# Kernel optimization log

Measured on AMD Instinct MI355X. Metric: run time of the kernel, lower is better.

Reference implementation:

```python
import jax, jax.numpy as jnp
import numpy as np

DT = 1e-3   # timestep (s)
DH = 10.0   # grid spacing (m)


def setup_inputs() -> dict:
    key = jax.random.key(0)
    k1, k2, k3, k4 = jax.random.split(key, 4)
    B, NT, NZ, NX, NREC = 8, 256, 256, 256, 64
    x = jax.random.normal(k1, (B, NT), dtype=jnp.float32)            # source wavelets
    vp = 1500.0 + 2000.0 * jax.random.uniform(k2, (NZ, NX), dtype=jnp.float32)
    src_loc = jax.random.randint(k3, (B, 2), 4, NZ - 4, dtype=jnp.int32)        # (z,x) per shot
    rec_loc = jax.random.randint(k4, (B, NREC, 2), 4, NZ - 4, dtype=jnp.int32)  # (z,x) per rec
    return {"x": x, "vp": vp, "src_loc": src_loc, "rec_loc": rec_loc}


def reference(x, vp, src_loc, rec_loc):
    """Acoustic 2nd-order leapfrog FD time-stepping (WaveRNN pattern):
    per step: stencil update -> source scatter-inject -> receiver gather.
    Returns receiver traces (B, NT, NREC)."""
    B, NT = x.shape
    nz, nx = vp.shape
    c2dt2 = (vp * vp) * jnp.float32(DT * DT)   # (nz, nx), broadcast over batch
    inv_dh2 = jnp.float32(1.0 / (DH * DH))
    bidx = jnp.arange(B)
    sz, sx = src_loc[:, 0], src_loc[:, 1]
    rz, rx = rec_loc[..., 0], rec_loc[..., 1]

    def laplacian(h):  # 5-point stencil, zero (Dirichlet) boundaries
        interior = (h[:, 2:, 1:-1] + h[:, :-2, 1:-1]
                    + h[:, 1:-1, 2:] + h[:, 1:-1, :-2]
                    - 4.0 * h[:, 1:-1, 1:-1]) * inv_dh2
        return jnp.zeros_like(h).at[:, 1:-1, 1:-1].set(interior)

    def step(carry, wav_t):
        h1, h2 = carry                              # fields at t, t-1
        hn = 2.0 * h1 - h2 + c2dt2 * laplacian(h1)  # leapfrog update
        hn = hn.at[bidx, sz, sx].add(jnp.float32(DT * DT) * wav_t)  # source inject
        rec = hn[bidx[:, None], rz, rx]             # receiver gather (B, NREC)
        return (hn, h1), rec

    h0 = jnp.zeros((B, nz, nx), dtype=x.dtype)
    _, recs = jax.lax.scan(step, (h0, h0), x.T)     # recs: (NT, B, NREC)
    return jnp.transpose(recs, (1, 0, 2))           # (B, NT, NREC)
```

## Files before the change

### kernel.cpp

```cpp
#include <hip/hip_runtime.h>

typedef float v4f __attribute__((ext_vector_type(4)));

namespace {
constexpr int B_     = 8;
constexpr int NT_    = 256;
constexpr int NX_    = 256;
constexpr int NREC_  = 64;
constexpr int PIECES = 16;
constexpr int IROWS  = 16;
constexpr int G      = 16;
constexpr int ROUNDS = NT_ / G;
constexpr int NB     = (IROWS + 2 * G) / 4;
constexpr int NTHR   = NB * 64;
constexpr int NBLK   = B_ * PIECES;
constexpr float DT2  = 1e-6f;
constexpr float KLAP = 1e-8f;
constexpr size_t FLAGS_BYTES = 4096;
constexpr int RCAP = 6;
}

__device__ __forceinline__ float dpp_shr1(float v) {
    return __int_as_float(__builtin_amdgcn_update_dpp(
        0, __float_as_int(v), 0x138 , 0xF, 0xF, true));
}
__device__ __forceinline__ float dpp_shl1(float v) {
    return __int_as_float(__builtin_amdgcn_update_dpp(
        0, __float_as_int(v), 0x130 , 0xF, 0xF, true));
}

__device__ __forceinline__ void store_v4_sys(float* p, v4f v) {
    asm volatile("global_store_dwordx4 %0, %1, off sc0 sc1"
                 :: "v"(p), "v"(v) : "memory");
}
__device__ __forceinline__ v4f load_v4_sys(const float* p) {
    v4f r;
    asm volatile("global_load_dwordx4 %0, %1, off sc0 sc1"
                 : "=v"(r) : "v"(p) : "memory");
    return r;
}

extern "C" __global__
__attribute__((amdgpu_flat_work_group_size(NTHR, NTHR), amdgpu_waves_per_eu(4, 4)))
void wave_reg_kernel(const float* __restrict__ x,
                     const float* __restrict__ vp,
                     const int* __restrict__ src_loc,
                     const int* __restrict__ rec_loc,
                     float* __restrict__ out,
                     int* __restrict__ flags,
                     float* __restrict__ gbuf)
{
    __shared__ float pub[3][2][NB][256];
    __shared__ int   prog[NB];
    __shared__ float wav[NT_];
    __shared__ float recbuf[G][NREC_];
    __shared__ unsigned char recown[NREC_];

    const int bid  = blockIdx.x;
    const int b    = bid & 7;
    const int p    = bid >> 3;
    const int blk  = b * PIECES + p;
    const int tid  = threadIdx.x;
    const int band = tid >> 6;
    const int lane = tid & 63;
    const int c0   = lane << 2;
    const int grt  = p * IROWS - G + (band << 2);

    const int cut = (band < 4) ? ((band << 2) + 3)
                  : ((band < 8) ? G : (47 - (band << 2)));

    if (tid < NT_) wav[tid] = x[b * NT_ + tid];
    if (tid < NREC_) {
        int rz = rec_loc[(b * NREC_ + tid) * 2 + 0];
        recown[tid] = (rz >= p * IROWS && rz < p * IROWS + IROWS) ? 1 : 0;
    }

    v4f cf[4], cf2[4];
#pragma unroll
    for (int i = 0; i < 4; ++i) {
        int gr = grt + i;
        int crow = gr < 0 ? 0 : (gr > 255 ? 255 : gr);
        bool rowok = (gr >= 1) && (gr <= 254);
        v4f vv = *(const v4f*)&vp[crow * NX_ + c0];
        float cc[4];
#pragma unroll
        for (int k = 0; k < 4; ++k) {
            int col = c0 + k;
            float vk = (k == 0) ? vv.x : (k == 1) ? vv.y : (k == 2) ? vv.z : vv.w;
            cc[k] = (rowok && col >= 1 && col <= 254) ? vk * vk * KLAP : 0.f;
        }
        cf[i].x = cc[0]; cf[i].y = cc[1]; cf[i].z = cc[2]; cf[i].w = cc[3];
        cf2[i].x = 2.f - 4.f * cc[0]; cf2[i].y = 2.f - 4.f * cc[1];
        cf2[i].z = 2.f - 4.f * cc[2]; cf2[i].w = 2.f - 4.f * cc[3];
    }

    const int sz = src_loc[b * 2 + 0], sx = src_loc[b * 2 + 1];
    const int si = sz - grt;
    const int sj = sx - c0;
    const bool has_src = ((unsigned)si < 4u) && ((unsigned)sj < 4u);
    const bool wave_has_src = __any(has_src);

    int rs[RCAP]; int rcnt = 0;
#pragma unroll 1
    for (int r = 0; r < NREC_; ++r) {
        int rz = rec_loc[(b * NREC_ + r) * 2 + 0];
        int rx = rec_loc[(b * NREC_ + r) * 2 + 1];
        int i = rz - grt, j = rx - c0;
        if (rz >= p * IROWS && rz < p * IROWS + IROWS &&
            (unsigned)i < 4u && (unsigned)j < 4u) {
            if (rcnt < RCAP) rs[rcnt] = (r << 4) | (i << 2) | j;
            ++rcnt;
        }
    }
    if (rcnt > RCAP) rcnt = RCAP;
    const bool wave_has_rec = __any(rcnt > 0);
    float* outb = out + (size_t)b * NT_ * NREC_;

    v4f A[4], Bv[4];
    {
        v4f z = {0.f, 0.f, 0.f, 0.f};
#pragma unroll
        for (int i = 0; i < 4; ++i) { A[i] = z; Bv[i] = z; }
    }

    *(v4f*)&pub[0][0][band][c0] = A[0];
    *(v4f*)&pub[0][1][band][c0] = A[3];
    if (lane == 0) prog[band] = 0;
    __syncthreads();

    auto gptr = [&](int e, int bk, int lvl, int rr) -> float* {
        return gbuf + ((((size_t)(e & 1) * NBLK + bk) * 2 + lvl) * 16 + rr) * 256;
    };

#define ROW(I, NV, SV) do {                                                   \
    float wv = dpp_shr1(C[I].w);       \
    float ev = dpp_shl1(C[I].x);      \
    v4f hn;                                                                   \
    { float sm = ((NV).x + (SV).x) + (wv     + C[I].y);                       \
      hn.x = fmaf(cf[I].x, sm, fmaf(cf2[I].x, C[I].x, -P[I].x)); }            \
    { float sm = ((NV).y + (SV).y) + (C[I].x + C[I].z);                       \
      hn.y = fmaf(cf[I].y, sm, fmaf(cf2[I].y, C[I].y, -P[I].y)); }            \
    { float sm = ((NV).z + (SV).z) + (C[I].y + C[I].w);                       \
      hn.z = fmaf(cf[I].z, sm, fmaf(cf2[I].z, C[I].z, -P[I].z)); }            \
    { float sm = ((NV).w + (SV).w) + (C[I].z + ev);                           \
      hn.w = fmaf(cf[I].w, sm, fmaf(cf2[I].w, C[I].w, -P[I].w)); }            \
    P[I] = hn;                                                                \
} while (0)

    auto step = [&](v4f (&C)[4], v4f (&P)[4], int t, int s3) {
        const int k = (t & (G - 1)) + 1;
        if (k > cut) return;
        const int nxt = (s3 == 2) ? 0 : s3 + 1;
        if (band > 0)
            while (__hip_atomic_load(&prog[band - 1], __ATOMIC_ACQUIRE,
                                     __HIP_MEMORY_SCOPE_WORKGROUP) < t)
                __builtin_amdgcn_s_sleep(1);
        if (band < NB - 1)
            while (__hip_atomic_load(&prog[band + 1], __ATOMIC_ACQUIRE,
                                     __HIP_MEMORY_SCOPE_WORKGROUP) < t)
                __builtin_amdgcn_s_sleep(1);
        v4f nn, ss;
        if (band > 0)      nn = *(const v4f*)&pub[s3][1][band - 1][c0];
        else               { nn.x = 0.f; nn.y = 0.f; nn.z = 0.f; nn.w = 0.f; }
        if (band < NB - 1) ss = *(const v4f*)&pub[s3][0][band + 1][c0];
        else               { ss.x = 0.f; ss.y = 0.f; ss.z = 0.f; ss.w = 0.f; }
        ROW(1, C[0], C[2]);
        ROW(2, C[1], C[3]);
        ROW(0, nn,   C[1]);
        ROW(3, C[2], ss);
        if (wave_has_src) {
            const float sv = DT2 * wav[t];
#pragma unroll
            for (int i = 0; i < 4; ++i) {
                if (has_src && si == i) {
                    if      (sj == 0) P[i].x += sv;
                    else if (sj == 1) P[i].y += sv;
                    else if (sj == 2) P[i].z += sv;
                    else              P[i].w += sv;
                }
            }
        }
        *(v4f*)&pub[nxt][0][band][c0] = P[0];
        *(v4f*)&pub[nxt][1][band][c0] = P[3];
        const int nv = (k == cut && cut < G) ? (t - k + 17)
                                             : (t + 1);
        if (lane == 0)
            __hip_atomic_store(&prog[band], nv, __ATOMIC_RELEASE,
                               __HIP_MEMORY_SCOPE_WORKGROUP);
        if (wave_has_rec) {
#pragma unroll
            for (int kk = 0; kk < RCAP; ++kk) {
                if (rcnt > kk) {
                    int pk = rs[kk];
                    int i = (pk >> 2) & 3, j = pk & 3, r = pk >> 4;
                    v4f t01 = (i & 1) ? P[1] : P[0];
                    v4f t23 = (i & 1) ? P[3] : P[2];
                    v4f rw  = (i & 2) ? t23 : t01;
                    float c01 = (j & 1) ? rw.y : rw.x;
                    float c23 = (j & 1) ? rw.w : rw.z;
                    recbuf[t & (G - 1)][r] = (j & 2) ? c23 : c01;
                }
            }
        }
    };

    auto publish_prev = [&](int e) {
        if (band >= 4 && band < 8) {
            int rr0 = (band - 4) << 2;
#pragma unroll
            for (int i = 0; i < 4; ++i)
                store_v4_sys(&gptr(e, blk, 1, rr0 + i)[c0], Bv[i]);
        }
    };

    auto exchange = [&](int e, int s3) {
        if (band >= 4 && band < 8) {
            int rr0 = (band - 4) << 2;
#pragma unroll
            for (int i = 0; i < 4; ++i)
                store_v4_sys(&gptr(e, blk, 0, rr0 + i)[c0], A[i]);
        }
        __syncthreads();
        if (tid == 0)
            __hip_atomic_store(&flags[blk], e + 1, __ATOMIC_RELAXED,
                               __HIP_MEMORY_SCOPE_SYSTEM);
        if (band < 4 && p > 0) {
            if (lane == 0)
                while (__hip_atomic_load(&flags[blk - 1], __ATOMIC_RELAXED,
                                         __HIP_MEMORY_SCOPE_SYSTEM) < e + 1)
                    __builtin_amdgcn_s_sleep(1);
            int rr0 = band << 2;
#pragma unroll
            for (int i = 0; i < 4; ++i) {
                A[i]  = load_v4_sys(&gptr(e, blk - 1, 0, rr0 + i)[c0]);
                Bv[i] = load_v4_sys(&gptr(e, blk - 1, 1, rr0 + i)[c0]);
            }
        }
        if (band >= 8 && p < PIECES - 1) {
            if (lane == 0)
                while (__hip_atomic_load(&flags[blk + 1], __ATOMIC_RELAXED,
                                         __HIP_MEMORY_SCOPE_SYSTEM) < e + 1)
                    __builtin_amdgcn_s_sleep(1);
            int rr0 = (band - 8) << 2;
#pragma unroll
            for (int i = 0; i < 4; ++i) {
                A[i]  = load_v4_sys(&gptr(e, blk + 1, 0, rr0 + i)[c0]);
                Bv[i] = load_v4_sys(&gptr(e, blk + 1, 1, rr0 + i)[c0]);
            }
        }
        asm volatile("s_waitcnt vmcnt(0)" ::: "memory");
        __builtin_amdgcn_sched_barrier(0);
        *(v4f*)&pub[s3][0][band][c0] = A[0];
        *(v4f*)&pub[s3][1][band][c0] = A[3];
        __syncthreads();
    };

    int t = 0, s3 = 0;
#pragma unroll 1
    for (int e = 0; e < ROUNDS; ++e) {
#pragma unroll 1
        for (int s = 0; s < G; s += 2) {
            step(A, Bv, t, s3);  s3 = (s3 == 2) ? 0 : s3 + 1;
            if (s == G - 2 && e < ROUNDS - 1)
                publish_prev(e);
            step(Bv, A, t + 1, s3); s3 = (s3 == 2) ? 0 : s3 + 1;
            t += 2;
        }
        __syncthreads();
#pragma unroll 1
        for (int idx = tid; idx < G * NREC_; idx += NTHR) {
            int s = idx >> 6, r = idx & 63;
            if (recown[r]) outb[(e * G + s) * NREC_ + r] = recbuf[s][r];
        }
        if (e < ROUNDS - 1) exchange(e, s3);
    }
#undef ROW
}

extern "C" void kernel_launch(void* const* d_in, const int* in_sizes, int n_in,
                              void* d_out, int out_size, void* d_ws, size_t ws_size,
                              hipStream_t stream) {
    const float* x   = (const float*)d_in[0];
    const float* vp  = (const float*)d_in[1];
    const int*   src = (const int*)d_in[2];
    const int*   rec = (const int*)d_in[3];
    float*       o   = (float*)d_out;
    int*   flags = (int*)d_ws;
    float* gbuf  = (float*)((char*)d_ws + FLAGS_BYTES);
    (void)hipMemsetAsync(d_ws, 0, FLAGS_BYTES, stream);
    hipLaunchKernelGGL(wave_reg_kernel, dim3(NBLK), dim3(NTHR), 0, stream,
                       x, vp, src, rec, o, flags, gbuf);
}
```

Baseline: 298.8 us.

## Replace block-wide round barriers with per-band flags and direct receiver stores

Removes the per-round __syncthreads and shared-memory receiver staging. Receivers are now written straight to global memory from the owning wave. Cross-block halo exchange moves from per-block flags to per-band flags, so each interior band publishes its state and each halo band waits only for its own source band. Halo bands resynchronise with their inner neighbour through the existing progress counters instead of a block barrier. This lets bands drift across round boundaries, at the cost of more complex flag and progress bookkeeping and scattered global receiver stores.

```diff
diff --git a/kernel.cpp b/kernel.cpp
--- a/kernel.cpp
+++ b/kernel.cpp
@@ -11,7 +11,7 @@
 constexpr int IROWS  = 16;
 constexpr int G      = 16;
 constexpr int ROUNDS = NT_ / G;
-constexpr int NB     = (IROWS + 2 * G) / 4;
+constexpr int NB     = 12;
 constexpr int NTHR   = NB * 64;
 constexpr int NBLK   = B_ * PIECES;
 constexpr float DT2  = 1e-6f;
@@ -53,8 +53,6 @@
     __shared__ float pub[3][2][NB][256];
     __shared__ int   prog[NB];
     __shared__ float wav[NT_];
-    __shared__ float recbuf[G][NREC_];
-    __shared__ unsigned char recown[NREC_];
 
     const int bid  = blockIdx.x;
     const int b    = bid & 7;
@@ -70,10 +68,6 @@
                   : ((band < 8) ? G : (47 - (band << 2)));
 
     if (tid < NT_) wav[tid] = x[b * NT_ + tid];
-    if (tid < NREC_) {
-        int rz = rec_loc[(b * NREC_ + tid) * 2 + 0];
-        recown[tid] = (rz >= p * IROWS && rz < p * IROWS + IROWS) ? 1 : 0;
-    }
 
     v4f cf[4], cf2[4];
 #pragma unroll
@@ -133,8 +127,8 @@
     };
 
 #define ROW(I, NV, SV) do {                                                   \
-    float wv = dpp_shr1(C[I].w);       \
-    float ev = dpp_shl1(C[I].x);      \
+    float wv = dpp_shr1(C[I].w);                                              \
+    float ev = dpp_shl1(C[I].x);                                              \
     v4f hn;                                                                   \
     { float sm = ((NV).x + (SV).x) + (wv     + C[I].y);                       \
       hn.x = fmaf(cf[I].x, sm, fmaf(cf2[I].x, C[I].x, -P[I].x)); }            \
@@ -147,9 +141,8 @@
     P[I] = hn;                                                                \
 } while (0)
 
-    auto step = [&](v4f (&C)[4], v4f (&P)[4], int t, int s3) {
-        const int k = (t & (G - 1)) + 1;
-        if (k > cut) return;
+    auto step = [&](v4f (&C)[4], v4f (&P)[4], int t) {
+        const int s3  = t % 3;
         const int nxt = (s3 == 2) ? 0 : s3 + 1;
         if (band > 0)
             while (__hip_atomic_load(&prog[band - 1], __ATOMIC_ACQUIRE,
@@ -182,10 +175,8 @@
         }
         *(v4f*)&pub[nxt][0][band][c0] = P[0];
         *(v4f*)&pub[nxt][1][band][c0] = P[3];
-        const int nv = (k == cut && cut < G) ? (t - k + 17)
-                                             : (t + 1);
         if (lane == 0)
-            __hip_atomic_store(&prog[band], nv, __ATOMIC_RELEASE,
+            __hip_atomic_store(&prog[band], t + 1, __ATOMIC_RELEASE,
                                __HIP_MEMORY_SCOPE_WORKGROUP);
         if (wave_has_rec) {
 #pragma unroll
@@ -198,81 +189,68 @@
                     v4f rw  = (i & 2) ? t23 : t01;
                     float c01 = (j & 1) ? rw.y : rw.x;
                     float c23 = (j & 1) ? rw.w : rw.z;
-                    recbuf[t & (G - 1)][r] = (j & 2) ? c23 : c01;
+                    outb[t * NREC_ + r] = (j & 2) ? c23 : c01;
                 }
             }
         }
     };
 
-    auto publish_prev = [&](int e) {
-        if (band >= 4 && band < 8) {
-            int rr0 = (band - 4) << 2;
-#pragma unroll
-            for (int i = 0; i < 4; ++i)
-                store_v4_sys(&gptr(e, blk, 1, rr0 + i)[c0], Bv[i]);
-        }
-    };
-
-    auto exchange = [&](int e, int s3) {
-        if (band >= 4 && band < 8) {
-            int rr0 = (band - 4) << 2;
-#pragma unroll
-            for (int i = 0; i < 4; ++i)
-                store_v4_sys(&gptr(e, blk, 0, rr0 + i)[c0], A[i]);
-        }
-        __syncthreads();
-        if (tid == 0)
-            __hip_atomic_store(&flags[blk], e + 1, __ATOMIC_RELAXED,
-                               __HIP_MEMORY_SCOPE_SYSTEM);
-        if (band < 4 && p > 0) {
+    int t0 = 0;
+#pragma unroll 1
+    for (int e = 0; e < ROUNDS; ++e, t0 += G) {
+#pragma unroll 1
+        for (int k = 1; k <= cut; k += 2) {
+            step(A, Bv, t0 + k - 1);
+            if (k < cut) step(Bv, A, t0 + k);
+        }
+        if (cut == G) {
+            if (e < ROUNDS - 1) {
+                int rr0 = (band - 4) << 2;
+#pragma unroll
+                for (int i = 0; i < 4; ++i) {
+                    store_v4_sys(&gptr(e, blk, 0, rr0 + i)[c0], A[i]);
+                    store_v4_sys(&gptr(e, blk, 1, rr0 + i)[c0], Bv[i]);
+                }
+                asm volatile("s_waitcnt vmcnt(0)" ::: "memory");
+                __hip_atomic_store(&flags[blk * 4 + (band - 4)], e + 1,
+                                   __ATOMIC_RELAXED, __HIP_MEMORY_SCOPE_SYSTEM);
+            }
+        } else {
             if (lane == 0)
-                while (__hip_atomic_load(&flags[blk - 1], __ATOMIC_RELAXED,
-                                         __HIP_MEMORY_SCOPE_SYSTEM) < e + 1)
+                __hip_atomic_store(&prog[band], t0 + 15, __ATOMIC_RELEASE,
+                                   __HIP_MEMORY_SCOPE_WORKGROUP);
+            if (e < ROUNDS - 1) {
+                const bool top    = band < 4;
+                const int  srcblk = top ? blk - 1 : blk + 1;
+                const bool have   = top ? (p > 0) : (p < PIECES - 1);
+                if (have) {
+                    const int fi = top ? band : band - 8;
+                    if (lane == 0)
+                        while (__hip_atomic_load(&flags[srcblk * 4 + fi],
+                                 __ATOMIC_RELAXED,
+                                 __HIP_MEMORY_SCOPE_SYSTEM) < e + 1)
+                            __builtin_amdgcn_s_sleep(1);
+                    const int rr0 = top ? (band << 2) : ((band - 8) << 2);
+#pragma unroll
+                    for (int i = 0; i < 4; ++i) {
+                        A[i]  = load_v4_sys(&gptr(e, srcblk, 0, rr0 + i)[c0]);
+                        Bv[i] = load_v4_sys(&gptr(e, srcblk, 1, rr0 + i)[c0]);
+                    }
+                    asm volatile("s_waitcnt vmcnt(0)" ::: "memory");
+                    __builtin_amdgcn_sched_barrier(0);
+                }
+                const int inn = top ? band + 1 : band - 1;
+                while (__hip_atomic_load(&prog[inn], __ATOMIC_ACQUIRE,
+                                         __HIP_MEMORY_SCOPE_WORKGROUP) < t0 + 14)
                     __builtin_amdgcn_s_sleep(1);
-            int rr0 = band << 2;
-#pragma unroll
-            for (int i = 0; i < 4; ++i) {
-                A[i]  = load_v4_sys(&gptr(e, blk - 1, 0, rr0 + i)[c0]);
-                Bv[i] = load_v4_sys(&gptr(e, blk - 1, 1, rr0 + i)[c0]);
-            }
-        }
-        if (band >= 8 && p < PIECES - 1) {
-            if (lane == 0)
-                while (__hip_atomic_load(&flags[blk + 1], __ATOMIC_RELAXED,
-                                         __HIP_MEMORY_SCOPE_SYSTEM) < e + 1)
-                    __builtin_amdgcn_s_sleep(1);
-            int rr0 = (band - 8) << 2;
-#pragma unroll
-            for (int i = 0; i < 4; ++i) {
-                A[i]  = load_v4_sys(&gptr(e, blk + 1, 0, rr0 + i)[c0]);
-                Bv[i] = load_v4_sys(&gptr(e, blk + 1, 1, rr0 + i)[c0]);
-            }
-        }
-        asm volatile("s_waitcnt vmcnt(0)" ::: "memory");
-        __builtin_amdgcn_sched_barrier(0);
-        *(v4f*)&pub[s3][0][band][c0] = A[0];
-        *(v4f*)&pub[s3][1][band][c0] = A[3];
-        __syncthreads();
-    };
-
-    int t = 0, s3 = 0;
-#pragma unroll 1
-    for (int e = 0; e < ROUNDS; ++e) {
-#pragma unroll 1
-        for (int s = 0; s < G; s += 2) {
-            step(A, Bv, t, s3);  s3 = (s3 == 2) ? 0 : s3 + 1;
-            if (s == G - 2 && e < ROUNDS - 1)
-                publish_prev(e);
-            step(Bv, A, t + 1, s3); s3 = (s3 == 2) ? 0 : s3 + 1;
-            t += 2;
-        }
-        __syncthreads();
-#pragma unroll 1
-        for (int idx = tid; idx < G * NREC_; idx += NTHR) {
-            int s = idx >> 6, r = idx & 63;
-            if (recown[r]) outb[(e * G + s) * NREC_ + r] = recbuf[s][r];
-        }
-        if (e < ROUNDS - 1) exchange(e, s3);
+                const int s3n = (t0 + G) % 3;
+                *(v4f*)&pub[s3n][0][band][c0] = A[0];
+                *(v4f*)&pub[s3n][1][band][c0] = A[3];
+                if (lane == 0)
+                    __hip_atomic_store(&prog[band], t0 + G, __ATOMIC_RELEASE,
+                                       __HIP_MEMORY_SCOPE_WORKGROUP);
+            }
+        }
     }
 #undef ROW
 }
```

Measured after the change: 342.4 us. +14.6%, slower.
